# Kernel tuning notes

Measured on AMD Instinct MI355X. Metric: run time of the kernel, lower is better.

Reference implementation:

```python
import jax, jax.numpy as jnp
import numpy as np

B = 131072    # batch of toy 2D points
H = 256       # effective hidden width (dims[1], = out_dims * group_card)
NB = 8        # n_blocks i-ResBlocks
NMID = 3      # middle layers: dims 2->256->256->256->256->2 => 1 in + 3 mid + 1 out
NPS = 5       # n_power_series terms for log-det trace estimator


def setup_inputs() -> dict:
    key = jax.random.key(0)
    ks = jax.random.split(key, 8)
    # small scales keep each g-net contractive (coeff<1 Lipschitz, as spectral norm would)
    x  = jax.random.normal(ks[0], (B, 2), jnp.float32)
    v  = jax.random.normal(ks[1], (B, 2), jnp.float32)  # Hutchinson probe (n_samples=1)
    Wi = jax.random.normal(ks[2], (NB, 2, H), jnp.float32) * 0.05
    bi = jax.random.normal(ks[3], (NB, H), jnp.float32) * 0.01
    Wm = jax.random.normal(ks[4], (NB, NMID, H, H), jnp.float32) * (0.05 / np.sqrt(H))
    bm = jax.random.normal(ks[5], (NB, NMID, H), jnp.float32) * 0.01
    Wo = jax.random.normal(ks[6], (NB, H, 2), jnp.float32) * (0.05 / np.sqrt(H))
    bo = jax.random.normal(ks[7], (NB, 2), jnp.float32) * 0.01
    return {"x": x, "v": v, "Wi": Wi, "bi": bi, "Wm": Wm, "bm": bm, "Wo": Wo, "bo": bo}


def _g(x, Wi, bi, Wm, bm, Wo, bo):
    # equivariant 3x3 convs on 1x1 spatial maps == channel-mixing linears;
    # build_nnet appends the activation after EVERY conv, including the last.
    h = jax.nn.relu(x @ Wi + bi)
    for j in range(Wm.shape[0]):
        h = jax.nn.relu(h @ Wm[j] + bm[j])
    return jax.nn.relu(h @ Wo + bo)


def _iresblock(x, v, Wi, bi, Wm, bm, Wo, bo):
    gfun = lambda xx: _g(xx, Wi, bi, Wm, bm, Wo, bo)
    gx = gfun(x)
    # log det(I + J_g) ~= sum_{k=1..n} (-1)^{k+1}/k * v^T J_g^k v  (power series, Hutchinson)
    w = v
    logdet = jnp.zeros((x.shape[0], 1), x.dtype)
    for k in range(1, NPS + 1):
        _, w = jax.jvp(gfun, (x,), (w,))          # w <- J_g @ w
        coef = ((-1.0) ** (k + 1)) / k
        logdet = logdet + coef * jnp.sum(w * v, axis=1, keepdims=True)
    return x + gx, logdet


def reference(x, v, Wi, bi, Wm, bm, Wo, bo):
    z = x
    delta_logp = jnp.zeros((x.shape[0], 1), x.dtype)  # SequentialFlow: logpx - logdet per block
    for b in range(NB):
        z, ld = _iresblock(z, v, Wi[b], bi[b], Wm[b], bm[b], Wo[b], bo[b])
        delta_logp = delta_logp - ld
    return z, delta_logp
```

## Files before the change

### kernel.cpp

```cpp
#include <hip/hip_runtime.h>
#include <hip/hip_bf16.h>

#define BATCH 131072
#define H 256
#define NBLK 8
#define NMID 3
#define MS 32
#define RT_N 6
#define NT 512

typedef __attribute__((ext_vector_type(8))) short short8;
typedef __attribute__((ext_vector_type(4))) float f32x4;

__device__ __forceinline__ unsigned pk2(float a, float b) {
    unsigned ua = __float_as_uint(a) + 0x8000u;
    unsigned ub = __float_as_uint(b) + 0x8000u;
    return __builtin_amdgcn_perm(ub, ua, 0x07060302u);
}

__global__ void pack_w_kernel(const float* __restrict__ Wm, unsigned short* __restrict__ Wp) {
    int o = blockIdx.x * blockDim.x + threadIdx.x;
    if (o >= NBLK * NMID * 8192) return;
    int lane  = o & 63;
    int T     = (o >> 6) & 15;
    int kk    = (o >> 10) & 7;
    int layer = o >> 13;
    int n  = (T >> 2) * 64 + (lane & 15) * 4 + (T & 3);
    int k0 = kk * 32 + (lane >> 4) * 8;
    const float* src = Wm + (size_t)layer * H * H;
    unsigned int w[4];
    #pragma unroll
    for (int jj = 0; jj < 4; ++jj)
        w[jj] = pk2(src[(size_t)(k0 + 2*jj) * H + n], src[(size_t)(k0 + 2*jj + 1) * H + n]);
    uint4 val; val.x = w[0]; val.y = w[1]; val.z = w[2]; val.w = w[3];
    ((uint4*)Wp)[o] = val;
}

__device__ __forceinline__ void epilogue_write(const f32x4 (&acc)[RT_N][2],
                                               const float* __restrict__ bias,
                                               unsigned short* __restrict__ Xs,
                                               int wave, int lane) {
    const int mcol = lane & 15, quad = lane >> 4;
    const int C  = (wave >> 1) * 64 + mcol * 4 + ((wave & 1) << 1);
    const float b0 = bias[C], b1 = bias[C + 1];
    const int kkx = C >> 5;
    const int qx  = (C >> 3) & 3;
    const int jb  = C & 7;
    #pragma unroll
    for (int g = 0; g < 2; ++g) {
        #pragma unroll
        for (int r = 0; r < 4; ++r) {
            float pre0 = acc[g][0][r] + b0;
            float pre1 = acc[g][1][r] + b1;
            bool m0 = pre0 > 0.0f, m1 = pre1 > 0.0f;
            float h0 = m0 ? pre0 : 0.0f,          h1 = m1 ? pre1 : 0.0f;
            float a0 = m0 ? acc[2+g][0][r] : 0.0f, a1 = m1 ? acc[2+g][1][r] : 0.0f;
            float t0 = m0 ? acc[4+g][0][r] : 0.0f, t1 = m1 ? acc[4+g][1][r] : 0.0f;
            int rowm = quad * 4 + r;
            int le   = qx * 16 + rowm;
            int scl  = le ^ ((le >> 3) & 7);
            int e0   = (((g * 8 + kkx) * 64 + scl) * 8) + jb;
            *(unsigned*)(Xs + e0)          = pk2(h0, h1);
            *(unsigned*)(Xs + e0 + 8192)   = pk2(a0, a1);
            *(unsigned*)(Xs + e0 + 16384)  = pk2(t0, t1);
        }
    }
}

__global__ __launch_bounds__(NT, 4)
void flow_kernel(const float* __restrict__ x, const float* __restrict__ v,
                 const float* __restrict__ Wi, const float* __restrict__ bi,
                 const float* __restrict__ bm, const float* __restrict__ Wo,
                 const float* __restrict__ bo,
                 const unsigned short* __restrict__ Wp,
                 float* __restrict__ out)
{
    __shared__ uint4 Xl4[RT_N * 8 * 64];
    __shared__ float zbuf[MS * 2];
    __shared__ float vbuf[MS * 2];

    unsigned short* Xs = (unsigned short*)Xl4;

    const int tid  = threadIdx.x;
    const int wave = tid >> 6;
    const int lane = tid & 63;
    const int mcol = lane & 15;
    const int quad = lane >> 4;
    const int s0   = blockIdx.x * MS;
    const int rl   = lane ^ ((lane >> 3) & 7);

    float dlp = 0.0f;
    if (tid < MS) {
        zbuf[tid*2+0] = x[(size_t)(s0+tid)*2+0];
        zbuf[tid*2+1] = x[(size_t)(s0+tid)*2+1];
        vbuf[tid*2+0] = v[(size_t)(s0+tid)*2+0];
        vbuf[tid*2+1] = v[(size_t)(s0+tid)*2+1];
    }
    __syncthreads();

    for (int b = 0; b < NBLK; ++b) {
        if (tid < 384) {
            int rt = tid >> 6, cl = tid & 63;
            int l = cl ^ ((cl >> 3) & 7);
            int m = l & 15, q = l >> 4;
            int st = rt >> 1;
            uint4 pk = {0u, 0u, 0u, 0u};
            if (q == 0) {
                if (st == 0) {
                    int s = ((rt & 1) << 4) | m;
                    pk.x = pk2(zbuf[s*2+0], zbuf[s*2+1]);
                } else if (st == 1) pk.x = 0x00003F80u;
                else                pk.x = 0x3F800000u;
            }
            Xl4[rt * 512 + cl] = pk;
        }
        __syncthreads();

        const float* Wi0 = Wi + (size_t)b * 2 * H;
        const float* Wi1 = Wi0 + H;
        {
            short8 b0f[2];
            #pragma unroll
            for (int ct = 0; ct < 2; ++ct) {
                short8 z = {0,0,0,0,0,0,0,0};
                if (lane < 16) {
                    int n = (wave >> 1) * 64 + lane * 4 + ((wave & 1) << 1) + ct;
                    unsigned p = pk2(Wi0[n], Wi1[n]);
                    z[0] = (short)(p & 0xFFFFu);
                    z[1] = (short)(p >> 16);
                }
                b0f[ct] = z;
            }
            f32x4 acc[RT_N][2];
            #pragma unroll
            for (int rt = 0; rt < RT_N; ++rt)
                #pragma unroll
                for (int ct = 0; ct < 2; ++ct)
                    acc[rt][ct] = (f32x4){0.f, 0.f, 0.f, 0.f};
            #pragma unroll
            for (int rt = 0; rt < RT_N; ++rt) {
                short8 af = ((const short8*)Xl4)[(rt * 8) * 64 + rl];
                #pragma unroll
                for (int ct = 0; ct < 2; ++ct)
                    acc[rt][ct] = __builtin_amdgcn_mfma_f32_16x16x32_bf16(af, b0f[ct], acc[rt][ct], 0, 0, 0);
            }
            __syncthreads();
            epilogue_write(acc, bi + (size_t)b * H, Xs, wave, lane);
            __syncthreads();
        }

        for (int li = 0; li < NMID; ++li) {
            const int layer = b * NMID + li;
            const short8* Bp  = ((const short8*)Wp) + (size_t)layer * 8192;
            const float* bias = bm + (size_t)layer * H;

            f32x4 acc[RT_N][2];
            #pragma unroll
            for (int rt = 0; rt < RT_N; ++rt)
                #pragma unroll
                for (int ct = 0; ct < 2; ++ct)
                    acc[rt][ct] = (f32x4){0.f, 0.f, 0.f, 0.f};

            #pragma unroll 2
            for (int kk = 0; kk < 8; ++kk) {
                short8 bf[2];
                #pragma unroll
                for (int ct = 0; ct < 2; ++ct)
                    bf[ct] = Bp[(kk*16 + wave*2 + ct)*64 + lane];
                #pragma unroll
                for (int rt = 0; rt < RT_N; ++rt) {
                    short8 af = ((const short8*)Xl4)[(rt*8 + kk)*64 + rl];
                    #pragma unroll
                    for (int ct = 0; ct < 2; ++ct)
                        acc[rt][ct] = __builtin_amdgcn_mfma_f32_16x16x32_bf16(af, bf[ct], acc[rt][ct], 0, 0, 0);
                }
            }
            __syncthreads();
            epilogue_write(acc, bias, Xs, wave, lane);
            __syncthreads();
        }

        const float* Wob = Wo + (size_t)b * H * 2;
        const float* bob = bo + (size_t)b * 2;
        {
            short8 b4 = {0,0,0,0,0,0,0,0};
            if (mcol < 2) {
                int kb = wave * 32 + quad * 8;
                #pragma unroll
                for (int jj = 0; jj < 4; ++jj) {
                    unsigned p = pk2(Wob[(kb + 2*jj) * 2 + mcol], Wob[(kb + 2*jj + 1) * 2 + mcol]);
                    b4[2*jj]   = (short)(p & 0xFFFFu);
                    b4[2*jj+1] = (short)(p >> 16);
                }
            }
            f32x4 accL[RT_N];
            #pragma unroll
            for (int rt = 0; rt < RT_N; ++rt) accL[rt] = (f32x4){0.f, 0.f, 0.f, 0.f};
            #pragma unroll
            for (int rt = 0; rt < RT_N; ++rt) {
                short8 a0 = ((const short8*)Xl4)[(rt*8 + wave)*64 + rl];
                accL[rt] = __builtin_amdgcn_mfma_f32_16x16x32_bf16(a0, b4, accL[rt], 0, 0, 0);
            }
            __syncthreads();
            float* part = (float*)Xl4;
            if (mcol < 2) {
                #pragma unroll
                for (int rt = 0; rt < RT_N; ++rt)
                    #pragma unroll
                    for (int r = 0; r < 4; ++r)
                        part[((rt*16 + quad*4 + r)*2 + mcol)*8 + wave] = accL[rt][r];
            }
            __syncthreads();
            float* res = part + 1536;
            if (tid < 192) {
                float4 p4 = ((const float4*)part)[tid*2];
                float4 q4 = ((const float4*)part)[tid*2 + 1];
                res[tid] = (p4.x + p4.y + p4.z + p4.w) + (q4.x + q4.y + q4.z + q4.w);
            }
            __syncthreads();
            if (tid < MS) {
                int g = tid >> 4, row = tid & 15;
                int base = (g * 16 + row) * 2;
                float SH0 = res[base], SH1 = res[base + 1];
                float SA0 = res[base + 64], SA1 = res[base + 65];
                float SB0 = res[base + 128], SB1 = res[base + 129];
                float pre0 = SH0 + bob[0], pre1 = SH1 + bob[1];
                bool  m0 = pre0 > 0.f,     m1 = pre1 > 0.f;
                float gx0 = m0 ? pre0 : 0.f, gx1 = m1 ? pre1 : 0.f;
                float J00 = m0 ? SA0 : 0.f;
                float J01 = m0 ? SB0 : 0.f;
                float J10 = m1 ? SA1 : 0.f;
                float J11 = m1 ? SB1 : 0.f;
                float v0 = vbuf[tid*2+0], v1 = vbuf[tid*2+1];
                float w0 = v0, w1 = v1, ld = 0.f;
                const float coef[5] = {1.f, -0.5f, 1.f/3.f, -0.25f, 0.2f};
                #pragma unroll
                for (int k = 0; k < 5; ++k) {
                    float nw0 = fmaf(J00, w0, J01 * w1);
                    float nw1 = fmaf(J10, w0, J11 * w1);
                    w0 = nw0; w1 = nw1;
                    ld = fmaf(coef[k], fmaf(w0, v0, w1 * v1), ld);
                }
                zbuf[tid*2+0] += gx0;
                zbuf[tid*2+1] += gx1;
                dlp -= ld;
            }
        }
        __syncthreads();
    }

    if (tid < MS) {
        out[(size_t)(s0+tid)*2+0] = zbuf[tid*2+0];
        out[(size_t)(s0+tid)*2+1] = zbuf[tid*2+1];
        out[(size_t)2*BATCH + s0 + tid] = dlp;
    }
}

extern "C" void kernel_launch(void* const* d_in, const int* in_sizes, int n_in,
                              void* d_out, int out_size, void* d_ws, size_t ws_size,
                              hipStream_t stream) {
    const float* x  = (const float*)d_in[0];
    const float* v  = (const float*)d_in[1];
    const float* Wi = (const float*)d_in[2];
    const float* bi = (const float*)d_in[3];
    const float* Wm = (const float*)d_in[4];
    const float* bm = (const float*)d_in[5];
    const float* Wo = (const float*)d_in[6];
    const float* bo = (const float*)d_in[7];
    unsigned short* Wp = (unsigned short*)d_ws;

    int nchunks = NBLK * NMID * 8192;
    pack_w_kernel<<<(nchunks + 255) / 256, 256, 0, stream>>>(Wm, Wp);
    flow_kernel<<<BATCH / MS, NT, 0, stream>>>(x, v, Wi, bi, bm, Wo, bo, Wp, (float*)d_out);
}
```

Before: 1.195 ms.

## Retile waves into 2x4 row/column groups with wider B reuse and swizzled LDS

Changes the per-wave MFMA tiling from all six row tiles by two column tiles to three row tiles (one row group) by four column tiles (one column group). Each wave now loads four B fragments per k-step and reuses them across three A loads, so fewer LDS A reads are issued per MFMA. The epilogue writes four contiguous columns as 64-bit stores with a float4 bias load. An extra XOR swizzle keyed on the k-tile parity is applied consistently on writes and reads to reduce LDS bank conflicts. The wider per-wave B footprint increases global loads per wave and may change register pressure.

```diff
diff --git a/kernel.cpp b/kernel.cpp
--- a/kernel.cpp
+++ b/kernel.cpp
@@ -36,34 +36,39 @@
     ((uint4*)Wp)[o] = val;
 }
 
-__device__ __forceinline__ void epilogue_write(const f32x4 (&acc)[RT_N][2],
+__device__ __forceinline__ void epilogue_write(const f32x4 (&acc)[3][4],
                                                const float* __restrict__ bias,
                                                unsigned short* __restrict__ Xs,
-                                               int wave, int lane) {
+                                               int rg, int cg, int lane) {
     const int mcol = lane & 15, quad = lane >> 4;
-    const int C  = (wave >> 1) * 64 + mcol * 4 + ((wave & 1) << 1);
-    const float b0 = bias[C], b1 = bias[C + 1];
-    const int kkx = C >> 5;
-    const int qx  = (C >> 3) & 3;
-    const int jb  = C & 7;
+    const int nb = cg * 64 + mcol * 4;
+    const float4 bv = *(const float4*)(bias + nb);
+    const int kkx = nb >> 5;
+    const int qx  = (nb >> 3) & 3;
+    const int jb  = nb & 7;
+    const int kx1 = kkx & 1;
     #pragma unroll
-    for (int g = 0; g < 2; ++g) {
+    for (int r = 0; r < 4; ++r) {
+        float pre[4], hv[4], ta[4], tb[4];
+        pre[0] = acc[0][0][r] + bv.x; pre[1] = acc[0][1][r] + bv.y;
+        pre[2] = acc[0][2][r] + bv.z; pre[3] = acc[0][3][r] + bv.w;
         #pragma unroll
-        for (int r = 0; r < 4; ++r) {
-            float pre0 = acc[g][0][r] + b0;
-            float pre1 = acc[g][1][r] + b1;
-            bool m0 = pre0 > 0.0f, m1 = pre1 > 0.0f;
-            float h0 = m0 ? pre0 : 0.0f,          h1 = m1 ? pre1 : 0.0f;
-            float a0 = m0 ? acc[2+g][0][r] : 0.0f, a1 = m1 ? acc[2+g][1][r] : 0.0f;
-            float t0 = m0 ? acc[4+g][0][r] : 0.0f, t1 = m1 ? acc[4+g][1][r] : 0.0f;
-            int rowm = quad * 4 + r;
-            int le   = qx * 16 + rowm;
-            int scl  = le ^ ((le >> 3) & 7);
-            int e0   = (((g * 8 + kkx) * 64 + scl) * 8) + jb;
-            *(unsigned*)(Xs + e0)          = pk2(h0, h1);
-            *(unsigned*)(Xs + e0 + 8192)   = pk2(a0, a1);
-            *(unsigned*)(Xs + e0 + 16384)  = pk2(t0, t1);
-        }
+        for (int c = 0; c < 4; ++c) {
+            bool mk = pre[c] > 0.0f;
+            hv[c] = mk ? pre[c]      : 0.0f;
+            ta[c] = mk ? acc[1][c][r] : 0.0f;
+            tb[c] = mk ? acc[2][c][r] : 0.0f;
+        }
+        int rowm = quad * 4 + r;
+        int le   = qx * 16 + rowm;
+        int scl  = (le ^ ((le >> 3) & 7)) ^ kx1;
+        int e0   = (((rg * 8 + kkx) * 64 + scl) * 8) + jb;
+        uint2 ph; ph.x = pk2(hv[0], hv[1]); ph.y = pk2(hv[2], hv[3]);
+        uint2 pa; pa.x = pk2(ta[0], ta[1]); pa.y = pk2(ta[2], ta[3]);
+        uint2 pb; pb.x = pk2(tb[0], tb[1]); pb.y = pk2(tb[2], tb[3]);
+        *(uint2*)(Xs + e0)          = ph;
+        *(uint2*)(Xs + e0 + 8192)   = pa;
+        *(uint2*)(Xs + e0 + 16384)  = pb;
     }
 }
 
@@ -86,6 +91,8 @@
     const int lane = tid & 63;
     const int mcol = lane & 15;
     const int quad = lane >> 4;
+    const int rg   = wave >> 2;
+    const int cg   = wave & 3;
     const int s0   = blockIdx.x * MS;
     const int rl   = lane ^ ((lane >> 3) & 7);
 
@@ -119,33 +126,34 @@
         const float* Wi0 = Wi + (size_t)b * 2 * H;
         const float* Wi1 = Wi0 + H;
         {
-            short8 b0f[2];
-            #pragma unroll
-            for (int ct = 0; ct < 2; ++ct) {
+            short8 b0f[4];
+            #pragma unroll
+            for (int ct = 0; ct < 4; ++ct) {
                 short8 z = {0,0,0,0,0,0,0,0};
                 if (lane < 16) {
-                    int n = (wave >> 1) * 64 + lane * 4 + ((wave & 1) << 1) + ct;
+                    int n = cg * 64 + lane * 4 + ct;
                     unsigned p = pk2(Wi0[n], Wi1[n]);
                     z[0] = (short)(p & 0xFFFFu);
                     z[1] = (short)(p >> 16);
                 }
                 b0f[ct] = z;
             }
-            f32x4 acc[RT_N][2];
-            #pragma unroll
-            for (int rt = 0; rt < RT_N; ++rt)
-                #pragma unroll
-                for (int ct = 0; ct < 2; ++ct)
-                    acc[rt][ct] = (f32x4){0.f, 0.f, 0.f, 0.f};
-            #pragma unroll
-            for (int rt = 0; rt < RT_N; ++rt) {
+            f32x4 acc[3][4];
+            #pragma unroll
+            for (int st = 0; st < 3; ++st)
+                #pragma unroll
+                for (int ct = 0; ct < 4; ++ct)
+                    acc[st][ct] = (f32x4){0.f, 0.f, 0.f, 0.f};
+            #pragma unroll
+            for (int st = 0; st < 3; ++st) {
+                int rt = st * 2 + rg;
                 short8 af = ((const short8*)Xl4)[(rt * 8) * 64 + rl];
                 #pragma unroll
-                for (int ct = 0; ct < 2; ++ct)
-                    acc[rt][ct] = __builtin_amdgcn_mfma_f32_16x16x32_bf16(af, b0f[ct], acc[rt][ct], 0, 0, 0);
-            }
-            __syncthreads();
-            epilogue_write(acc, bi + (size_t)b * H, Xs, wave, lane);
+                for (int ct = 0; ct < 4; ++ct)
+                    acc[st][ct] = __builtin_amdgcn_mfma_f32_16x16x32_bf16(af, b0f[ct], acc[st][ct], 0, 0, 0);
+            }
+            __syncthreads();
+            epilogue_write(acc, bi + (size_t)b * H, Xs, rg, cg, lane);
             __syncthreads();
         }
 
@@ -154,29 +162,31 @@
             const short8* Bp  = ((const short8*)Wp) + (size_t)layer * 8192;
             const float* bias = bm + (size_t)layer * H;
 
-            f32x4 acc[RT_N][2];
-            #pragma unroll
-            for (int rt = 0; rt < RT_N; ++rt)
-                #pragma unroll
-                for (int ct = 0; ct < 2; ++ct)
-                    acc[rt][ct] = (f32x4){0.f, 0.f, 0.f, 0.f};
+            f32x4 acc[3][4];
+            #pragma unroll
+            for (int st = 0; st < 3; ++st)
+                #pragma unroll
+                for (int ct = 0; ct < 4; ++ct)
+                    acc[st][ct] = (f32x4){0.f, 0.f, 0.f, 0.f};
 
             #pragma unroll 2
             for (int kk = 0; kk < 8; ++kk) {
-                short8 bf[2];
-                #pragma unroll
-                for (int ct = 0; ct < 2; ++ct)
-                    bf[ct] = Bp[(kk*16 + wave*2 + ct)*64 + lane];
-                #pragma unroll
-                for (int rt = 0; rt < RT_N; ++rt) {
-                    short8 af = ((const short8*)Xl4)[(rt*8 + kk)*64 + rl];
+                short8 bf[4];
+                #pragma unroll
+                for (int ct = 0; ct < 4; ++ct)
+                    bf[ct] = Bp[(kk*16 + cg*4 + ct)*64 + lane];
+                const int rls = rl ^ (kk & 1);
+                #pragma unroll
+                for (int st = 0; st < 3; ++st) {
+                    int rt = st * 2 + rg;
+                    short8 af = ((const short8*)Xl4)[(rt*8 + kk)*64 + rls];
                     #pragma unroll
-                    for (int ct = 0; ct < 2; ++ct)
-                        acc[rt][ct] = __builtin_amdgcn_mfma_f32_16x16x32_bf16(af, bf[ct], acc[rt][ct], 0, 0, 0);
-                }
-            }
-            __syncthreads();
-            epilogue_write(acc, bias, Xs, wave, lane);
+                    for (int ct = 0; ct < 4; ++ct)
+                        acc[st][ct] = __builtin_amdgcn_mfma_f32_16x16x32_bf16(af, bf[ct], acc[st][ct], 0, 0, 0);
+                }
+            }
+            __syncthreads();
+            epilogue_write(acc, bias, Xs, rg, cg, lane);
             __syncthreads();
         }
 
@@ -196,9 +206,10 @@
             f32x4 accL[RT_N];
             #pragma unroll
             for (int rt = 0; rt < RT_N; ++rt) accL[rt] = (f32x4){0.f, 0.f, 0.f, 0.f};
+            const int rls = rl ^ (wave & 1);
             #pragma unroll
             for (int rt = 0; rt < RT_N; ++rt) {
-                short8 a0 = ((const short8*)Xl4)[(rt*8 + wave)*64 + rl];
+                short8 a0 = ((const short8*)Xl4)[(rt*8 + wave)*64 + rls];
                 accL[rt] = __builtin_amdgcn_mfma_f32_16x16x32_bf16(a0, b4, accL[rt], 0, 0, 0);
             }
             __syncthreads();
```

New measurement: 1.190 ms. Within noise of the previous version (-0.5%).
